# Kernel tuning notes

Hardware: AMD Instinct MI355X
Metric: run time of the kernel (lower is better)

## Reference

```python
import jax, jax.numpy as jnp
import numpy as np

T_STEPS = 100
T_EMB = 16
EPS = 1e-8


def sin_emb(t, dim):
    # sinusoidal_time_embedding: [cos(t*f), sin(t*f)] with f = exp(-log(1e4)*i/half)
    half = dim // 2
    freqs = jnp.exp(-jnp.log(jnp.float32(10000.0)) * jnp.arange(half, dtype=jnp.float32) / half)
    a = t.astype(jnp.float32)[:, None] * freqs[None, :]
    return jnp.concatenate([jnp.cos(a), jnp.sin(a)], axis=-1)


def lstm_layer(x_tbf, W_ih, W_hh, b):
    # x_tbf: [T, B, F]; torch gate order i, f, g, o
    B = x_tbf.shape[1]
    H = W_hh.shape[1]

    def step(carry, x_t):
        h, c = carry
        g = x_t @ W_ih.T + h @ W_hh.T + b
        i, f, gg, o = jnp.split(g, 4, axis=-1)
        c = jax.nn.sigmoid(f) * c + jax.nn.sigmoid(i) * jnp.tanh(gg)
        h = jax.nn.sigmoid(o) * jnp.tanh(c)
        return (h, c), h

    z = jnp.zeros((B, H), x_tbf.dtype)
    (h, c), ys = jax.lax.scan(step, (z, z), x_tbf)
    return ys, h


def _forward(x_hist, x_future, y0, turb_idx, pred_steps, init_noise, turb_emb,
             W_ih0, W_hh0, b_ih0, b_hh0, W_ih1, W_hh1, b_ih1, b_hh1,
             W1, b1, W2, b2, W3, b3):
    betas = jnp.linspace(1e-4, 0.02, T_STEPS).astype(jnp.float32)
    alphas = 1.0 - betas
    alpha_bars = jnp.cumprod(alphas)

    B = x_hist.shape[0]
    emb = turb_emb[turb_idx]  # [B, E]
    eh = jnp.broadcast_to(emb[:, None, :], (B, x_hist.shape[1], emb.shape[1]))
    ef = jnp.broadcast_to(emb[:, None, :], (B, x_future.shape[1], emb.shape[1]))
    xh = jnp.concatenate([x_hist, eh], axis=-1).transpose(1, 0, 2)    # [T_in, B, F+E]
    xf = jnp.concatenate([x_future, ef], axis=-1).transpose(1, 0, 2)  # [P, B, exo+E]

    ys0, _ = lstm_layer(xh, W_ih0, W_hh0, b_ih0 + b_hh0)
    _, enc_out = lstm_layer(ys0, W_ih1, W_hh1, b_ih1 + b_hh1)         # [B, H] = h[-1]

    def mlp(x):
        h = jax.nn.relu(x @ W1.T + b1)
        h = jax.nn.relu(h @ W2.T + b2)
        return h @ W3.T + b3

    def ar_step(prev_y, xs):
        exo_t, step, y_init = xs
        cond = jnp.concatenate([enc_out, exo_t, prev_y], axis=1)  # [B, cond_dim]
        h_e = sin_emb(jnp.full((B,), step), T_EMB)

        def dstep(y, t):
            t_e = sin_emb(jnp.full((B,), t), T_EMB)
            eps_hat = mlp(jnp.concatenate([cond, y, t_e, h_e], axis=1))  # [B,1]
            b_t, a_t, ab_t = betas[t], alphas[t], alpha_bars[t]
            pred_x0 = (y - jnp.sqrt(1.0 - ab_t) * eps_hat) / (jnp.sqrt(ab_t) + EPS)
            mean = (y - b_t / (jnp.sqrt(1.0 - ab_t) + EPS) * eps_hat) / (jnp.sqrt(a_t) + EPS)
            # eval mode -> deterministic sampling: posterior noise term is zero
            return jnp.where(t == 0, pred_x0, mean), None

        y, _ = jax.lax.scan(dstep, y_init, jnp.arange(T_STEPS - 1, -1, -1))
        return y, y[:, 0]

    _, seq = jax.lax.scan(ar_step, y0, (xf, jnp.arange(pred_steps), init_noise))
    return seq.T[:, :, None]  # [B, pred_steps, 1]


def setup_inputs() -> dict:
    key = jax.random.key(0)
    ks = list(jax.random.split(key, 24))
    kit = iter(ks)
    B, T_IN, F_IN, EXO, EMB, PRED, HID, NTURB = 1024, 96, 8, 6, 16, 8, 128, 100
    in0 = F_IN + EMB                 # 24
    cond_dim = HID + EXO + EMB + 1   # 151
    in_mlp = cond_dim + 1 + T_EMB + T_EMB  # 184

    def nrm(shape, s=0.05):
        return jax.random.normal(next(kit), shape, jnp.float32) * s

    return {
        'x_hist': jax.random.normal(next(kit), (B, T_IN, F_IN), jnp.float32),
        'x_future': jax.random.normal(next(kit), (B, PRED, EXO), jnp.float32),
        'y0': jnp.zeros((B, 1), jnp.float32),
        'turb_idx': jax.random.randint(next(kit), (B,), 0, NTURB),
        'pred_steps': PRED,
        'init_noise': jax.random.normal(next(kit), (PRED, B, 1), jnp.float32),
        'turb_emb': nrm((NTURB, EMB), 0.1),
        'W_ih0': nrm((4 * HID, in0)), 'W_hh0': nrm((4 * HID, HID)),
        'b_ih0': jnp.zeros((4 * HID,), jnp.float32), 'b_hh0': jnp.zeros((4 * HID,), jnp.float32),
        'W_ih1': nrm((4 * HID, HID)), 'W_hh1': nrm((4 * HID, HID)),
        'b_ih1': jnp.zeros((4 * HID,), jnp.float32), 'b_hh1': jnp.zeros((4 * HID,), jnp.float32),
        'W1': nrm((HID, in_mlp)), 'b1': jnp.zeros((HID,), jnp.float32),
        'W2': nrm((HID, HID)), 'b2': jnp.zeros((HID,), jnp.float32),
        'W3': nrm((1, HID)), 'b3': jnp.zeros((1,), jnp.float32),
    }


def reference(x_hist, x_future, y0, turb_idx, pred_steps, init_noise, turb_emb,
              W_ih0, W_hh0, b_ih0, b_hh0, W_ih1, W_hh1, b_ih1, b_hh1,
              W1, b1, W2, b2, W3, b3):
    return _forward(x_hist, x_future, y0, turb_idx, pred_steps, init_noise, turb_emb,
                    W_ih0, W_hh0, b_ih0, b_hh0, W_ih1, W_hh1, b_ih1, b_hh1,
                    W1, b1, W2, b2, W3, b3)
```

## Files before the change

kernel.cpp:

```cpp
#include <hip/hip_runtime.h>
#include <hip/hip_fp16.h>
#include <stdint.h>


typedef __attribute__((ext_vector_type(2))) _Float16 half2_t;
typedef __attribute__((ext_vector_type(8))) _Float16 v8h;
typedef __attribute__((ext_vector_type(4))) float v4f;

#define DEV __device__ __forceinline__

DEV uint32_t pack2f(float a, float b) {
  __half ha = __float2half_rn(a), hb = __float2half_rn(b);
  return (uint32_t)__half_as_ushort(ha) | ((uint32_t)__half_as_ushort(hb) << 16);
}

DEV float2 up2(uint32_t u) {
  half2_t h = __builtin_bit_cast(half2_t, u);
  return make_float2((float)h.x, (float)h.y);
}

DEV float fast_ex2(float x) {
#if __has_builtin(__builtin_amdgcn_exp2f)
  return __builtin_amdgcn_exp2f(x);
#else
  return exp2f(x);
#endif
}
DEV float fast_rcp(float x) {
#if __has_builtin(__builtin_amdgcn_rcpf)
  return __builtin_amdgcn_rcpf(x);
#else
  return 1.f / x;
#endif
}
DEV float sigm(float x) { return fast_rcp(1.f + fast_ex2(-1.4426950408889634f * x)); }
DEV float tanh_f(float x) {
  return 2.f * fast_rcp(1.f + fast_ex2(-2.8853900817779268f * x)) - 1.f;
}

DEV uint32_t pk_add(uint32_t a, uint32_t b) {
  return __builtin_bit_cast(uint32_t,
      __builtin_bit_cast(half2_t, a) + __builtin_bit_cast(half2_t, b));
}

DEV uint32_t pk_relufma(uint32_t w, uint32_t y, uint32_t b) {
  half2_t r = __builtin_bit_cast(half2_t, w) * __builtin_bit_cast(half2_t, y) +
              __builtin_bit_cast(half2_t, b);
  half2_t z = {(_Float16)0.f, (_Float16)0.f};
#if __has_builtin(__builtin_elementwise_max)
  r = __builtin_elementwise_max(r, z);
#else
  uint32_t u = __builtin_bit_cast(uint32_t, r);
  uint32_t mask = ((u >> 15) & 1u) * 0xFFFFu | ((u >> 31) & 1u) * 0xFFFF0000u;
  r = __builtin_bit_cast(half2_t, u & ~mask);
#endif
  return __builtin_bit_cast(uint32_t, r);
}

DEV uint32_t pk_max0(uint32_t a) {
  half2_t z = {(_Float16)0.f, (_Float16)0.f};
#if __has_builtin(__builtin_elementwise_max)
  return __builtin_bit_cast(uint32_t,
      __builtin_elementwise_max(__builtin_bit_cast(half2_t, a), z));
#else
  uint32_t mask = ((a >> 15) & 1u) * 0xFFFFu | ((a >> 31) & 1u) * 0xFFFF0000u;
  return a & ~mask;
#endif
}

DEV uint32_t cvtpk(float y) {
#if __has_builtin(__builtin_amdgcn_cvt_pkrtz)
  return __builtin_bit_cast(uint32_t, __builtin_amdgcn_cvt_pkrtz(y, y));
#else
  return pack2f(y, y);
#endif
}

DEV uint32_t cvtpk2(float a, float b) {
#if __has_builtin(__builtin_amdgcn_cvt_pkrtz)
  return __builtin_bit_cast(uint32_t, __builtin_amdgcn_cvt_pkrtz(a, b));
#else
  return pack2f(a, b);
#endif
}

DEV half2_t pk_fma2(uint32_t a, uint32_t b, half2_t c) {
  return __builtin_bit_cast(half2_t, a) * __builtin_bit_cast(half2_t, b) + c;
}

static constexpr size_t OFF_XH  = 0;
static constexpr size_t OFF_W0  = 4718592;
static constexpr size_t OFF_BS0 = 4882432;
static constexpr size_t OFF_W1L = 4884480;
static constexpr size_t OFF_BS1 = 5146624;
static constexpr size_t OFF_W2P = 5148672;
static constexpr size_t OFF_ENC = 5181440;
static constexpr size_t OFF_YS0 = 5705728;
static constexpr size_t OFF_TPJ = 30871552;
static constexpr size_t OFF_HPJ = 30897152;
static constexpr size_t OFF_CC  = 30899200;

__global__ void k_prep_xh(const float* __restrict__ xh, const int* __restrict__ tix,
                          const float* __restrict__ temb, uint32_t* __restrict__ out) {
  int idx = blockIdx.x * 256 + threadIdx.x;
  if (idx >= 96 * 1024 * 12) return;
  int m = idx % 12;
  int tb = idx / 12;
  int b = tb & 1023, t = tb >> 10;
  int k0 = 2 * m, k1 = k0 + 1;
  float v0 = (k0 < 8) ? xh[(b * 96 + t) * 8 + k0] : temb[tix[b] * 16 + (k0 - 8)];
  float v1 = (k1 < 8) ? xh[(b * 96 + t) * 8 + k1] : temb[tix[b] * 16 + (k1 - 8)];
  out[idx] = pack2f(v0, v1);
}

__global__ void k_prep_w(const float* __restrict__ Wih0, const float* __restrict__ Whh0,
                         const float* __restrict__ bih0, const float* __restrict__ bhh0,
                         const float* __restrict__ Wih1, const float* __restrict__ Whh1,
                         const float* __restrict__ bih1, const float* __restrict__ bhh1,
                         const float* __restrict__ W2, const float* __restrict__ W1,
                         uint32_t* __restrict__ w0p, uint32_t* __restrict__ w1p,
                         uint32_t* __restrict__ w2p, float* __restrict__ bs0,
                         float* __restrict__ bs1, uint32_t* __restrict__ tpj,
                         uint32_t* __restrict__ hpj, float2* __restrict__ ccg) {
  int idx = blockIdx.x * 256 + threadIdx.x;
  if (idx < 40960) {
    int w = idx / 5120;
    int r = idx % 5120;
    int T = r / 1280; r %= 1280;
    int f = r / 256;  r %= 256;
    int l = r >> 2, c = r & 3;
    int m = l & 15, qf = l >> 4;
    int g = (m & 3) * 128 + w * 16 + (m >> 2) * 4 + T;
    int k0 = f * 32 + qf * 8 + 2 * c, k1 = k0 + 1;
    float a = (k0 < 24) ? Wih0[g * 24 + k0] : ((k0 < 152) ? Whh0[g * 128 + k0 - 24] : 0.f);
    float b = (k1 < 24) ? Wih0[g * 24 + k1] : ((k1 < 152) ? Whh0[g * 128 + k1 - 24] : 0.f);
    w0p[idx] = pack2f(a, b);
  } else if (idx < 106496) {
    int i = idx - 40960;
    int w = i / 8192;
    int r = i % 8192;
    int T = r / 2048; r %= 2048;
    int f = r / 256;  r %= 256;
    int l = r >> 2, c = r & 3;
    int m = l & 15, qf = l >> 4;
    int g = (m & 3) * 128 + w * 16 + (m >> 2) * 4 + T;
    int k0 = f * 32 + qf * 8 + 2 * c, k1 = k0 + 1;
    float a = (k0 < 128) ? Wih1[g * 128 + k0] : Whh1[g * 128 + k0 - 128];
    float b = (k1 < 128) ? Wih1[g * 128 + k1] : Whh1[g * 128 + k1 - 128];
    w1p[i] = pack2f(a, b);
  } else if (idx < 114688) {
    int i = idx - 106496;
    w2p[i] = pack2f(W2[2 * i], W2[2 * i + 1]);
  } else if (idx < 115200) {
    int i = idx - 114688;
    bs0[i] = bih0[i] + bhh0[i];
  } else if (idx < 115712) {
    int i = idx - 115200;
    bs1[i] = bih1[i] + bhh1[i];
  } else if (idx < 122112) {
    int i = idx - 115712;
    int t = i / 64;
    int r = i % 64;
    int q = r / 16, pi = r % 16;
    int k0 = (pi >> 2) * 32 + q * 8 + (pi & 3) * 2;
    float te[16];
#pragma unroll
    for (int j = 0; j < 8; j++) {
      float f = expf(-logf(10000.f) * (float)j / 8.f);
      float a = (float)t * f;
      te[j] = cosf(a);
      te[j + 8] = sinf(a);
    }
    float s0 = 0.f, s1 = 0.f;
#pragma unroll
    for (int j = 0; j < 16; j++) {
      s0 += W1[k0 * 184 + 152 + j] * te[j];
      s1 += W1[(k0 + 1) * 184 + 152 + j] * te[j];
    }
    tpj[i] = pack2f((float)__half2float(__float2half_rn(s0)),
                    (float)__half2float(__float2half_rn(s1)));
  } else if (idx < 122624) {
    int i = idx - 122112;
    int s = i / 64;
    int kp = i % 64;
    float te[16];
#pragma unroll
    for (int j = 0; j < 8; j++) {
      float f = expf(-logf(10000.f) * (float)j / 8.f);
      float a = (float)s * f;
      te[j] = cosf(a);
      te[j + 8] = sinf(a);
    }
    float s0 = 0.f, s1 = 0.f;
#pragma unroll
    for (int j = 0; j < 16; j++) {
      s0 += W1[(2 * kp) * 184 + 168 + j] * te[j];
      s1 += W1[(2 * kp + 1) * 184 + 168 + j] * te[j];
    }
    hpj[i] = pack2f((float)__half2float(__float2half_rn(s0)),
                    (float)__half2float(__float2half_rn(s1)));
  } else if (idx < 122724) {
    int qq = idx - 122624;
    float ab = 1.f, beta = 0.f;
    for (int i = 0; i <= qq; i++) {
      beta = 1e-4f + (0.02f - 1e-4f) * (float)i / 99.f;
      ab *= (1.f - beta);
    }
    float cs, cd;
    if (qq == 0) { cs = sqrtf(1.f - ab); cd = 1.f / (sqrtf(ab) + 1e-8f); }
    else { cs = beta / (sqrtf(1.f - ab) + 1e-8f); cd = 1.f / (sqrtf(1.f - beta) + 1e-8f); }
    ccg[qq] = make_float2(cs, cd);
  }
}

__global__ __launch_bounds__(512, 2) void k_lstm0(const uint32_t* __restrict__ xh16,
                                                  const uint32_t* __restrict__ w0A,
                                                  const float* __restrict__ bs0,
                                                  __half* __restrict__ ys0) {
  __shared__ __align__(16) __half inb[2][16][160];
  const int tid = threadIdx.x;
  const int w = tid >> 6, l = tid & 63;
  const int n = l & 15, ql = l >> 4;
  const int ju = w * 16 + ql * 4;
  const int bbase = blockIdx.x * 16;

  uint4 Af[4][5];
#pragma unroll
  for (int T = 0; T < 4; T++)
#pragma unroll
    for (int f = 0; f < 5; f++)
      Af[T][f] = ((const uint4*)w0A)[((w * 4 + T) * 5 + f) * 64 + l];
  float bias[4][4];
#pragma unroll
  for (int T = 0; T < 4; T++)
#pragma unroll
    for (int r = 0; r < 4; r++) bias[T][r] = bs0[r * 128 + ju + T];

  for (int i = tid; i < 2560; i += 512) ((uint32_t*)inb)[i] = 0u;
  __syncthreads();
  if (tid < 192) {
    int b = tid / 12, m = tid % 12;
    ((uint32_t*)&inb[0][b][0])[m] = xh16[(0 * 1024 + bbase + b) * 12 + m];
  }
  float cst[4] = {0.f, 0.f, 0.f, 0.f};
  __syncthreads();

  for (int t = 0; t < 96; t++) {
    const int cur = t & 1, nxt = cur ^ 1;
    uint32_t sx = 0;
    int sb = 0, sm = 0;
    if (t < 95 && tid < 192) {
      sb = tid / 12; sm = tid % 12;
      sx = xh16[((t + 1) * 1024 + bbase + sb) * 12 + sm];
    }
    v4f acc[4];
#pragma unroll
    for (int T = 0; T < 4; T++) acc[T] = (v4f){0.f, 0.f, 0.f, 0.f};
#pragma unroll
    for (int f = 0; f < 5; f++) {
      uint4 bu = *(const uint4*)&inb[cur][n][f * 32 + ql * 8];
      v8h Bv = __builtin_bit_cast(v8h, bu);
#pragma unroll
      for (int T = 0; T < 4; T++)
        acc[T] = __builtin_amdgcn_mfma_f32_16x16x32_f16(
            __builtin_bit_cast(v8h, Af[T][f]), Bv, acc[T], 0, 0, 0);
    }
    float hv[4];
#pragma unroll
    for (int T = 0; T < 4; T++) {
      float gi = acc[T][0] + bias[T][0];
      float gf = acc[T][1] + bias[T][1];
      float gg = acc[T][2] + bias[T][2];
      float go = acc[T][3] + bias[T][3];
      float c = sigm(gf) * cst[T] + sigm(gi) * tanh_f(gg);
      cst[T] = c;
      hv[T] = sigm(go) * tanh_f(c);
    }
    uint32_t h01 = pack2f(hv[0], hv[1]), h23 = pack2f(hv[2], hv[3]);
    *(uint2*)&inb[nxt][n][24 + ju] = make_uint2(h01, h23);
    *(uint2*)((__half*)ys0 + (size_t)(t * 1024 + bbase + n) * 128 + ju) = make_uint2(h01, h23);
    if (t < 95 && tid < 192) ((uint32_t*)&inb[nxt][sb][0])[sm] = sx;
    __syncthreads();
  }
}

__global__ __launch_bounds__(512, 2) void k_lstm1(const uint32_t* __restrict__ ys0u,
                                                  const uint32_t* __restrict__ w1A,
                                                  const float* __restrict__ bs1,
                                                  float* __restrict__ enc) {
  __shared__ __align__(16) __half inb[2][16][264];
  const int tid = threadIdx.x;
  const int w = tid >> 6, l = tid & 63;
  const int n = l & 15, ql = l >> 4;
  const int ju = w * 16 + ql * 4;
  const int bbase = blockIdx.x * 16;
  const int sb = tid >> 5, sc = tid & 31;

  uint4 Af[4][8];
#pragma unroll
  for (int T = 0; T < 4; T++)
#pragma unroll
    for (int f = 0; f < 8; f++)
      Af[T][f] = ((const uint4*)w1A)[((w * 4 + T) * 8 + f) * 64 + l];
  float bias[4][4];
#pragma unroll
  for (int T = 0; T < 4; T++)
#pragma unroll
    for (int r = 0; r < 4; r++) bias[T][r] = bs1[r * 128 + ju + T];

  for (int i = tid; i < 4224; i += 512) ((uint32_t*)inb)[i] = 0u;
  __syncthreads();
  {
    uint2 v = ((const uint2*)ys0u)[(size_t)(0 * 1024 + bbase + sb) * 32 + sc];
    *(uint2*)&inb[0][sb][sc * 4] = v;
  }
  float cst[4] = {0.f, 0.f, 0.f, 0.f};
  __syncthreads();

  for (int t = 0; t < 96; t++) {
    const int cur = t & 1, nxt = cur ^ 1;
    uint2 sv = make_uint2(0u, 0u);
    if (t < 95)
      sv = ((const uint2*)ys0u)[(size_t)((t + 1) * 1024 + bbase + sb) * 32 + sc];
    v4f acc[4];
#pragma unroll
    for (int T = 0; T < 4; T++) acc[T] = (v4f){0.f, 0.f, 0.f, 0.f};
#pragma unroll
    for (int f = 0; f < 8; f++) {
      uint4 bu = *(const uint4*)&inb[cur][n][f * 32 + ql * 8];
      v8h Bv = __builtin_bit_cast(v8h, bu);
#pragma unroll
      for (int T = 0; T < 4; T++)
        acc[T] = __builtin_amdgcn_mfma_f32_16x16x32_f16(
            __builtin_bit_cast(v8h, Af[T][f]), Bv, acc[T], 0, 0, 0);
    }
    float hv[4];
#pragma unroll
    for (int T = 0; T < 4; T++) {
      float gi = acc[T][0] + bias[T][0];
      float gf = acc[T][1] + bias[T][1];
      float gg = acc[T][2] + bias[T][2];
      float go = acc[T][3] + bias[T][3];
      float c = sigm(gf) * cst[T] + sigm(gi) * tanh_f(gg);
      cst[T] = c;
      hv[T] = sigm(go) * tanh_f(c);
    }
    *(uint2*)&inb[nxt][n][128 + ju] = make_uint2(pack2f(hv[0], hv[1]), pack2f(hv[2], hv[3]));
    if (t < 95) *(uint2*)&inb[nxt][sb][sc * 4] = sv;
    if (t == 95)
      *(float4*)&enc[(size_t)(bbase + n) * 128 + ju] = make_float4(hv[0], hv[1], hv[2], hv[3]);
    __syncthreads();
  }
}

__global__ __launch_bounds__(128, 1) void k_diff(
    const float* __restrict__ xfut, const float* __restrict__ y0,
    const int* __restrict__ tix, const float* __restrict__ noise,
    const float* __restrict__ temb, const float* __restrict__ W1,
    const float* __restrict__ b1, const float* __restrict__ b2,
    const float* __restrict__ W3, const float* __restrict__ b3,
    const uint32_t* __restrict__ w2p, const float* __restrict__ enc,
    const uint32_t* __restrict__ tpj, const uint32_t* __restrict__ hpj,
    const float2* __restrict__ ccG, float* __restrict__ out) {
  __shared__ uint32_t W1sL[128 * 65];
  __shared__ uint32_t W1xL[128 * 29];
  __shared__ uint32_t encPL[16 * 65];
  __shared__ uint32_t embPL[16 * 9];
  __shared__ uint32_t encdL[128 * 17];
  __shared__ __align__(16) float partL[2][16][12];

  const int tid = threadIdx.x;
  const int w = tid >> 6, l = tid & 63;
  const int m = l & 15, q = l >> 4;
  const int gbase = blockIdx.x * 16;
  const uint4* tpj4 = (const uint4*)tpj;

  for (int i = tid; i < 128 * 64; i += 128) {
    int r = i >> 6, c = i & 63;
    W1sL[r * 65 + c] = pack2f(W1[r * 184 + 2 * c], W1[r * 184 + 2 * c + 1]);
  }
  for (int i = tid; i < 128 * 28; i += 128) {
    int r = i / 28, c = i % 28;
    W1xL[r * 29 + c] = pack2f(W1[r * 184 + 128 + 2 * c], W1[r * 184 + 129 + 2 * c]);
  }
  for (int i = tid; i < 16 * 64; i += 128) {
    int bq = i >> 6, c = i & 63;
    encPL[bq * 65 + c] = pack2f(enc[(gbase + bq) * 128 + 2 * c],
                                enc[(gbase + bq) * 128 + 2 * c + 1]);
  }
  for (int i = tid; i < 16 * 8; i += 128) {
    int bq = i >> 3, c = i & 7;
    const float* er = temb + tix[gbase + bq] * 16;
    embPL[bq * 9 + c] = pack2f(er[2 * c], er[2 * c + 1]);
  }
  __syncthreads();

  for (int pi = 0; pi < 16; pi++) {
    int k0 = (pi >> 2) * 32 + q * 8 + (pi & 3) * 2;
    half2_t a0 = {(_Float16)0.f, (_Float16)0.f};
    half2_t a1 = a0;
    const uint32_t* wr0 = &W1sL[k0 * 65];
    const uint32_t* wr1 = &W1sL[(k0 + 1) * 65];
    const uint32_t* ep = &encPL[m * 65];
#pragma unroll 8
    for (int c = 0; c < 64; c++) {
      half2_t e = __builtin_bit_cast(half2_t, ep[c]);
      a0 += __builtin_bit_cast(half2_t, wr0[c]) * e;
      a1 += __builtin_bit_cast(half2_t, wr1[c]) * e;
    }
#pragma unroll
    for (int c = 0; c < 8; c++) {
      half2_t e = __builtin_bit_cast(half2_t, embPL[m * 9 + c]);
      a0 += __builtin_bit_cast(half2_t, W1xL[k0 * 29 + 3 + c]) * e;
      a1 += __builtin_bit_cast(half2_t, W1xL[(k0 + 1) * 29 + 3 + c]) * e;
    }
    float e0 = b1[k0] + (float)a0.x + (float)a0.y;
    float e1 = b1[k0 + 1] + (float)a1.x + (float)a1.y;
    encdL[tid * 17 + pi] = pack2f(e0, e1);
  }

  uint4 Bf[4][4];
  {
    const uint4* w2u4 = (const uint4*)w2p;
#pragma unroll
    for (int j = 0; j < 4; j++)
#pragma unroll
      for (int f = 0; f < 4; f++)
        Bf[j][f] = w2u4[((4 * w + j) * 16 + m) * 16 + f * 4 + q];
  }
  uint32_t b2P[8], w3P[8];
#pragma unroll
  for (int j = 0; j < 4; j++) {
    int tt = 4 * w + j;
    b2P[2 * j]     = pack2f(b2[tt * 16 + q * 4 + 0], b2[tt * 16 + q * 4 + 1]);
    b2P[2 * j + 1] = pack2f(b2[tt * 16 + q * 4 + 2], b2[tt * 16 + q * 4 + 3]);
    w3P[2 * j]     = pack2f(W3[tt * 16 + q * 4 + 0], W3[tt * 16 + q * 4 + 1]);
    w3P[2 * j + 1] = pack2f(W3[tt * 16 + q * 4 + 2], W3[tt * 16 + q * 4 + 3]);
  }
  const float b3v = b3[0];
  const int pslot = w * 4 + q;

  uint32_t w1yP[16];
#pragma unroll
  for (int pi = 0; pi < 16; pi++) {
    int k0 = (pi >> 2) * 32 + q * 8 + (pi & 3) * 2;
    uint32_t ua = W1xL[k0 * 29 + 11];
    uint32_t ub = W1xL[(k0 + 1) * 29 + 11];
    w1yP[pi] = (ua >> 16) | (ub & 0xFFFF0000u);
  }

  float prev_y = y0[gbase + m];
  __syncthreads();

  float y = 0.f;
  float2 ccv = make_float2(0.f, 0.f);
  uint32_t bph[16], bt[16];
  const v4f zf = (v4f){0.f, 0.f, 0.f, 0.f};

#define DSTEP(t_, PB)                                                          \
  do {                                                                         \
    const int tn_ = ((t_) > 0) ? (t_) - 1 : 0;                                 \
    const uint4* tg_ = tpj4 + (size_t)(tn_ * 4 + q) * 4;    \
    uint4 t0 = tg_[0], t1 = tg_[1], t2 = tg_[2], t3 = tg_[3];                  \
    float2 ccn_ = ccG[tn_];                                                    \
    const uint32_t yP = cvtpk(y);                                              \
    uint4 au[4];                                                               \
    _Pragma("unroll")                                                          \
    for (int f = 0; f < 4; f++) {                                              \
      au[f].x = pk_relufma(w1yP[4 * f + 0], yP, bt[4 * f + 0]);                \
      au[f].y = pk_relufma(w1yP[4 * f + 1], yP, bt[4 * f + 1]);                \
      au[f].z = pk_relufma(w1yP[4 * f + 2], yP, bt[4 * f + 2]);                \
      au[f].w = pk_relufma(w1yP[4 * f + 3], yP, bt[4 * f + 3]);                \
    }                                                                          \
                            \
    v4f aA[4], aB[4];                                                          \
    _Pragma("unroll")                                                          \
    for (int j = 0; j < 4; j++)                                                \
      aA[j] = __builtin_amdgcn_mfma_f32_16x16x32_f16(                          \
          __builtin_bit_cast(v8h, Bf[j][0]), __builtin_bit_cast(v8h, au[0]),   \
          zf, 0, 0, 0);                                                        \
    _Pragma("unroll")                                                          \
    for (int j = 0; j < 4; j++)                                                \
      aB[j] = __builtin_amdgcn_mfma_f32_16x16x32_f16(                          \
          __builtin_bit_cast(v8h, Bf[j][1]), __builtin_bit_cast(v8h, au[1]),   \
          zf, 0, 0, 0);                                                        \
    _Pragma("unroll")                                                          \
    for (int j = 0; j < 4; j++)                                                \
      aA[j] = __builtin_amdgcn_mfma_f32_16x16x32_f16(                          \
          __builtin_bit_cast(v8h, Bf[j][2]), __builtin_bit_cast(v8h, au[2]),   \
          aA[j], 0, 0, 0);                                                     \
    _Pragma("unroll")                                                          \
    for (int j = 0; j < 4; j++)                                                \
      aB[j] = __builtin_amdgcn_mfma_f32_16x16x32_f16(                          \
          __builtin_bit_cast(v8h, Bf[j][3]), __builtin_bit_cast(v8h, au[3]),   \
          aB[j], 0, 0, 0);                                                     \
              \
    half2_t runA = {(_Float16)0.f, (_Float16)0.f};                             \
    half2_t runB = runA;                                                       \
    _Pragma("unroll")                                                          \
    for (int j = 0; j < 2; j++) {                                              \
      v4f c = aA[j] + aB[j];                                                   \
      uint32_t h01 = pk_max0(pk_add(cvtpk2(c[0], c[1]), b2P[2 * j]));          \
      uint32_t h23 = pk_max0(pk_add(cvtpk2(c[2], c[3]), b2P[2 * j + 1]));      \
      runA = pk_fma2(h01, w3P[2 * j], runA);                                   \
      runA = pk_fma2(h23, w3P[2 * j + 1], runA);                               \
    }                                                                          \
    _Pragma("unroll")                                                          \
    for (int j = 2; j < 4; j++) {                                              \
      v4f c = aA[j] + aB[j];                                                   \
      uint32_t h01 = pk_max0(pk_add(cvtpk2(c[0], c[1]), b2P[2 * j]));          \
      uint32_t h23 = pk_max0(pk_add(cvtpk2(c[2], c[3]), b2P[2 * j + 1]));      \
      runB = pk_fma2(h01, w3P[2 * j], runB);                                   \
      runB = pk_fma2(h23, w3P[2 * j + 1], runB);                               \
    }                                                                          \
    partL[PB][m][pslot] = ((float)runA.x + (float)runA.y) +                    \
                          ((float)runB.x + (float)runB.y);                     \
                                         \
    bt[0] = pk_add(bph[0], t0.x);   bt[1] = pk_add(bph[1], t0.y);              \
    bt[2] = pk_add(bph[2], t0.z);   bt[3] = pk_add(bph[3], t0.w);              \
    bt[4] = pk_add(bph[4], t1.x);   bt[5] = pk_add(bph[5], t1.y);              \
    bt[6] = pk_add(bph[6], t1.z);   bt[7] = pk_add(bph[7], t1.w);              \
    bt[8] = pk_add(bph[8], t2.x);   bt[9] = pk_add(bph[9], t2.y);              \
    bt[10] = pk_add(bph[10], t2.z); bt[11] = pk_add(bph[11], t2.w);            \
    bt[12] = pk_add(bph[12], t3.x); bt[13] = pk_add(bph[13], t3.y);            \
    bt[14] = pk_add(bph[14], t3.z); bt[15] = pk_add(bph[15], t3.w);            \
    __syncthreads();                                                           \
    const v4f* pl_ = (const v4f*)&partL[PB][m][0];                             \
    v4f ps_ = pl_[0] + pl_[1];                                                 \
    float eps_ = b3v + ((ps_[0] + ps_[1]) + (ps_[2] + ps_[3]));                \
    y = (y - ccv.x * eps_) * ccv.y;                                            \
    ccv = ccn_;                                                                \
  } while (0)

  for (int s = 0; s < 8; s++) {
    float yn = noise[s * 1024 + gbase + m];
    float xf[6];
#pragma unroll
    for (int i = 0; i < 6; i++) xf[i] = xfut[((gbase + m) * 8 + s) * 6 + i];
#pragma unroll
    for (int pi = 0; pi < 16; pi++) {
      int k0 = (pi >> 2) * 32 + q * 8 + (pi & 3) * 2;
      float2 ed = up2(encdL[tid * 17 + pi]);
      float e0 = ed.x, e1 = ed.y;
#pragma unroll
      for (int c = 0; c < 3; c++) {
        float2 w0v = up2(W1xL[k0 * 29 + c]);
        float2 w1v = up2(W1xL[(k0 + 1) * 29 + c]);
        e0 += w0v.x * xf[2 * c] + w0v.y * xf[2 * c + 1];
        e1 += w1v.x * xf[2 * c] + w1v.y * xf[2 * c + 1];
      }
      e0 += up2(W1xL[k0 * 29 + 11]).x * prev_y;
      e1 += up2(W1xL[(k0 + 1) * 29 + 11]).x * prev_y;
      float2 hh = up2(hpj[s * 64 + (k0 >> 1)]);
      e0 += hh.x;
      e1 += hh.y;
      bph[pi] = pack2f(e0, e1);
    }

    y = yn;
    {
      const uint4* tg = tpj4 + (size_t)(99 * 4 + q) * 4;
      uint4 t0 = tg[0], t1 = tg[1], t2 = tg[2], t3 = tg[3];
      bt[0] = pk_add(bph[0], t0.x);   bt[1] = pk_add(bph[1], t0.y);
      bt[2] = pk_add(bph[2], t0.z);   bt[3] = pk_add(bph[3], t0.w);
      bt[4] = pk_add(bph[4], t1.x);   bt[5] = pk_add(bph[5], t1.y);
      bt[6] = pk_add(bph[6], t1.z);   bt[7] = pk_add(bph[7], t1.w);
      bt[8] = pk_add(bph[8], t2.x);   bt[9] = pk_add(bph[9], t2.y);
      bt[10] = pk_add(bph[10], t2.z); bt[11] = pk_add(bph[11], t2.w);
      bt[12] = pk_add(bph[12], t3.x); bt[13] = pk_add(bph[13], t3.y);
      bt[14] = pk_add(bph[14], t3.z); bt[15] = pk_add(bph[15], t3.w);
    }
    ccv = ccG[99];

    for (int it = 0; it < 50; it++) {
      DSTEP(99 - 2 * it, 0);
      DSTEP(98 - 2 * it, 1);
    }

    if (w == 0 && l < 16) out[(gbase + l) * 8 + s] = y;
    prev_y = y;
  }
#undef DSTEP
}

extern "C" void kernel_launch(void* const* d_in, const int* in_sizes, int n_in,
                              void* d_out, int out_size, void* d_ws, size_t ws_size,
                              hipStream_t stream) {
  const float* x_hist    = (const float*)d_in[0];
  const float* x_future  = (const float*)d_in[1];
  const float* y0        = (const float*)d_in[2];
  const int*   turb_idx  = (const int*)d_in[3];
  const float* init_noise = (const float*)d_in[5];
  const float* turb_emb  = (const float*)d_in[6];
  const float* W_ih0     = (const float*)d_in[7];
  const float* W_hh0     = (const float*)d_in[8];
  const float* b_ih0     = (const float*)d_in[9];
  const float* b_hh0     = (const float*)d_in[10];
  const float* W_ih1     = (const float*)d_in[11];
  const float* W_hh1     = (const float*)d_in[12];
  const float* b_ih1     = (const float*)d_in[13];
  const float* b_hh1     = (const float*)d_in[14];
  const float* W1        = (const float*)d_in[15];
  const float* b1        = (const float*)d_in[16];
  const float* W2        = (const float*)d_in[17];
  const float* b2        = (const float*)d_in[18];
  const float* W3        = (const float*)d_in[19];
  const float* b3        = (const float*)d_in[20];

  char* ws = (char*)d_ws;
  uint32_t* xh16 = (uint32_t*)(ws + OFF_XH);
  uint32_t* w0p  = (uint32_t*)(ws + OFF_W0);
  float*    bs0  = (float*)(ws + OFF_BS0);
  uint32_t* w1p  = (uint32_t*)(ws + OFF_W1L);
  float*    bs1  = (float*)(ws + OFF_BS1);
  uint32_t* w2p  = (uint32_t*)(ws + OFF_W2P);
  float*    encf = (float*)(ws + OFF_ENC);
  __half*   ys0h = (__half*)(ws + OFF_YS0);
  uint32_t* tpjw = (uint32_t*)(ws + OFF_TPJ);
  uint32_t* hpjw = (uint32_t*)(ws + OFF_HPJ);
  float2*   ccw  = (float2*)(ws + OFF_CC);

  k_prep_xh<<<4608, 256, 0, stream>>>(x_hist, turb_idx, turb_emb, xh16);
  k_prep_w<<<480, 256, 0, stream>>>(W_ih0, W_hh0, b_ih0, b_hh0,
                                    W_ih1, W_hh1, b_ih1, b_hh1,
                                    W2, W1, w0p, w1p, w2p, bs0, bs1,
                                    tpjw, hpjw, ccw);
  k_lstm0<<<64, 512, 0, stream>>>(xh16, w0p, bs0, ys0h);
  k_lstm1<<<64, 512, 0, stream>>>((const uint32_t*)ys0h, w1p, bs1, encf);
  k_diff<<<64, 128, 0, stream>>>(x_future, y0, turb_idx, init_noise, turb_emb,
                                 W1, b1, b2, W3, b3, w2p, encf,
                                 tpjw, hpjw, ccw, (float*)d_out);
}
```

Measured before the change: 702.0 us.

## Split diffusion MLP output tiles across four waves and fold step coefficients

The diffusion kernel moves from 2 to 4 waves per block. Each wave now computes 2 of the 8 output column tiles of the second MLP layer instead of 4, which halves the serial MFMA chain and the register footprint per wave, with partial sums reduced through a wider shared buffer. The update coefficients are also prefolded (cs*cd), so the y update is a precomputed term minus a scaled sum and work moves off the post-barrier critical path. The cost is more waves joining each per-step barrier and a 16-way shared-memory reduction instead of 8-way.

New measurement: 633.2 us (median of 2 runs). 9.8% less time.

```diff
diff --git a/kernel.cpp b/kernel.cpp
--- a/kernel.cpp
+++ b/kernel.cpp
@@ -209,7 +209,7 @@
     float cs, cd;
     if (qq == 0) { cs = sqrtf(1.f - ab); cd = 1.f / (sqrtf(ab) + 1e-8f); }
     else { cs = beta / (sqrtf(1.f - ab) + 1e-8f); cd = 1.f / (sqrtf(1.f - beta) + 1e-8f); }
-    ccg[qq] = make_float2(cs, cd);
+    ccg[qq] = make_float2(cs * cd, cd);
   }
 }
 
@@ -353,7 +353,7 @@
   }
 }
 
-__global__ __launch_bounds__(128, 1) void k_diff(
+__global__ __launch_bounds__(256, 1) void k_diff(
     const float* __restrict__ xfut, const float* __restrict__ y0,
     const int* __restrict__ tix, const float* __restrict__ noise,
     const float* __restrict__ temb, const float* __restrict__ W1,
@@ -366,8 +366,8 @@
   __shared__ uint32_t W1xL[128 * 29];
   __shared__ uint32_t encPL[16 * 65];
   __shared__ uint32_t embPL[16 * 9];
-  __shared__ uint32_t encdL[128 * 17];
-  __shared__ __align__(16) float partL[2][16][12];
+  __shared__ uint32_t encdL[256 * 17];
+  __shared__ __align__(16) float partL[2][16][20];
 
   const int tid = threadIdx.x;
   const int w = tid >> 6, l = tid & 63;
@@ -375,20 +375,20 @@
   const int gbase = blockIdx.x * 16;
   const uint4* tpj4 = (const uint4*)tpj;
 
-  for (int i = tid; i < 128 * 64; i += 128) {
+  for (int i = tid; i < 128 * 64; i += 256) {
     int r = i >> 6, c = i & 63;
     W1sL[r * 65 + c] = pack2f(W1[r * 184 + 2 * c], W1[r * 184 + 2 * c + 1]);
   }
-  for (int i = tid; i < 128 * 28; i += 128) {
+  for (int i = tid; i < 128 * 28; i += 256) {
     int r = i / 28, c = i % 28;
     W1xL[r * 29 + c] = pack2f(W1[r * 184 + 128 + 2 * c], W1[r * 184 + 129 + 2 * c]);
   }
-  for (int i = tid; i < 16 * 64; i += 128) {
+  for (int i = tid; i < 16 * 64; i += 256) {
     int bq = i >> 6, c = i & 63;
     encPL[bq * 65 + c] = pack2f(enc[(gbase + bq) * 128 + 2 * c],
                                 enc[(gbase + bq) * 128 + 2 * c + 1]);
   }
-  for (int i = tid; i < 16 * 8; i += 128) {
+  for (int i = tid; i < 16 * 8; i += 256) {
     int bq = i >> 3, c = i & 7;
     const float* er = temb + tix[gbase + bq] * 16;
     embPL[bq * 9 + c] = pack2f(er[2 * c], er[2 * c + 1]);
@@ -419,19 +419,19 @@
     encdL[tid * 17 + pi] = pack2f(e0, e1);
   }
 
-  uint4 Bf[4][4];
+  uint4 Bf[2][4];
   {
     const uint4* w2u4 = (const uint4*)w2p;
 #pragma unroll
-    for (int j = 0; j < 4; j++)
+    for (int j = 0; j < 2; j++)
 #pragma unroll
       for (int f = 0; f < 4; f++)
-        Bf[j][f] = w2u4[((4 * w + j) * 16 + m) * 16 + f * 4 + q];
-  }
-  uint32_t b2P[8], w3P[8];
-#pragma unroll
-  for (int j = 0; j < 4; j++) {
-    int tt = 4 * w + j;
+        Bf[j][f] = w2u4[((2 * w + j) * 16 + m) * 16 + f * 4 + q];
+  }
+  uint32_t b2P[4], w3P[4];
+#pragma unroll
+  for (int j = 0; j < 2; j++) {
+    int tt = 2 * w + j;
     b2P[2 * j]     = pack2f(b2[tt * 16 + q * 4 + 0], b2[tt * 16 + q * 4 + 1]);
     b2P[2 * j + 1] = pack2f(b2[tt * 16 + q * 4 + 2], b2[tt * 16 + q * 4 + 3]);
     w3P[2 * j]     = pack2f(W3[tt * 16 + q * 4 + 0], W3[tt * 16 + q * 4 + 1]);
@@ -462,7 +462,7 @@
     const int tn_ = ((t_) > 0) ? (t_) - 1 : 0;                                 \
     const uint4* tg_ = tpj4 + (size_t)(tn_ * 4 + q) * 4;    \
     uint4 t0 = tg_[0], t1 = tg_[1], t2 = tg_[2], t3 = tg_[3];                  \
-    float2 ccn_ = ccG[tn_];                                                    \
+    float2 cck_ = ccG[tn_];                                                    \
     const uint32_t yP = cvtpk(y);                                              \
     uint4 au[4];                                                               \
     _Pragma("unroll")                                                          \
@@ -472,50 +472,44 @@
       au[f].z = pk_relufma(w1yP[4 * f + 2], yP, bt[4 * f + 2]);                \
       au[f].w = pk_relufma(w1yP[4 * f + 3], yP, bt[4 * f + 3]);                \
     }                                                                          \
-                            \
-    v4f aA[4], aB[4];                                                          \
-    _Pragma("unroll")                                                          \
-    for (int j = 0; j < 4; j++)                                                \
-      aA[j] = __builtin_amdgcn_mfma_f32_16x16x32_f16(                          \
-          __builtin_bit_cast(v8h, Bf[j][0]), __builtin_bit_cast(v8h, au[0]),   \
-          zf, 0, 0, 0);                                                        \
-    _Pragma("unroll")                                                          \
-    for (int j = 0; j < 4; j++)                                                \
-      aB[j] = __builtin_amdgcn_mfma_f32_16x16x32_f16(                          \
-          __builtin_bit_cast(v8h, Bf[j][1]), __builtin_bit_cast(v8h, au[1]),   \
-          zf, 0, 0, 0);                                                        \
-    _Pragma("unroll")                                                          \
-    for (int j = 0; j < 4; j++)                                                \
-      aA[j] = __builtin_amdgcn_mfma_f32_16x16x32_f16(                          \
-          __builtin_bit_cast(v8h, Bf[j][2]), __builtin_bit_cast(v8h, au[2]),   \
-          aA[j], 0, 0, 0);                                                     \
-    _Pragma("unroll")                                                          \
-    for (int j = 0; j < 4; j++)                                                \
-      aB[j] = __builtin_amdgcn_mfma_f32_16x16x32_f16(                          \
-          __builtin_bit_cast(v8h, Bf[j][3]), __builtin_bit_cast(v8h, au[3]),   \
-          aB[j], 0, 0, 0);                                                     \
-              \
+                             \
+    v4f a0 = __builtin_amdgcn_mfma_f32_16x16x32_f16(                           \
+        __builtin_bit_cast(v8h, Bf[0][0]), __builtin_bit_cast(v8h, au[0]), zf, 0, 0, 0); \
+    v4f b0 = __builtin_amdgcn_mfma_f32_16x16x32_f16(                           \
+        __builtin_bit_cast(v8h, Bf[0][1]), __builtin_bit_cast(v8h, au[1]), zf, 0, 0, 0); \
+    v4f a1 = __builtin_amdgcn_mfma_f32_16x16x32_f16(                           \
+        __builtin_bit_cast(v8h, Bf[1][0]), __builtin_bit_cast(v8h, au[0]), zf, 0, 0, 0); \
+    v4f b1x = __builtin_amdgcn_mfma_f32_16x16x32_f16(                          \
+        __builtin_bit_cast(v8h, Bf[1][1]), __builtin_bit_cast(v8h, au[1]), zf, 0, 0, 0); \
+    a0 = __builtin_amdgcn_mfma_f32_16x16x32_f16(                               \
+        __builtin_bit_cast(v8h, Bf[0][2]), __builtin_bit_cast(v8h, au[2]), a0, 0, 0, 0); \
+    b0 = __builtin_amdgcn_mfma_f32_16x16x32_f16(                               \
+        __builtin_bit_cast(v8h, Bf[0][3]), __builtin_bit_cast(v8h, au[3]), b0, 0, 0, 0); \
+    a1 = __builtin_amdgcn_mfma_f32_16x16x32_f16(                               \
+        __builtin_bit_cast(v8h, Bf[1][2]), __builtin_bit_cast(v8h, au[2]), a1, 0, 0, 0); \
+    b1x = __builtin_amdgcn_mfma_f32_16x16x32_f16(                              \
+        __builtin_bit_cast(v8h, Bf[1][3]), __builtin_bit_cast(v8h, au[3]), b1x, 0, 0, 0); \
+    v4f c0 = a0 + b0, c1 = a1 + b1x;                                           \
+                      \
     half2_t runA = {(_Float16)0.f, (_Float16)0.f};                             \
     half2_t runB = runA;                                                       \
-    _Pragma("unroll")                                                          \
-    for (int j = 0; j < 2; j++) {                                              \
-      v4f c = aA[j] + aB[j];                                                   \
-      uint32_t h01 = pk_max0(pk_add(cvtpk2(c[0], c[1]), b2P[2 * j]));          \
-      uint32_t h23 = pk_max0(pk_add(cvtpk2(c[2], c[3]), b2P[2 * j + 1]));      \
-      runA = pk_fma2(h01, w3P[2 * j], runA);                                   \
-      runA = pk_fma2(h23, w3P[2 * j + 1], runA);                               \
-    }                                                                          \
-    _Pragma("unroll")                                                          \
-    for (int j = 2; j < 4; j++) {                                              \
-      v4f c = aA[j] + aB[j];                                                   \
-      uint32_t h01 = pk_max0(pk_add(cvtpk2(c[0], c[1]), b2P[2 * j]));          \
-      uint32_t h23 = pk_max0(pk_add(cvtpk2(c[2], c[3]), b2P[2 * j + 1]));      \
-      runB = pk_fma2(h01, w3P[2 * j], runB);                                   \
-      runB = pk_fma2(h23, w3P[2 * j + 1], runB);                               \
+    {                                                                          \
+      uint32_t h01 = pk_max0(pk_add(cvtpk2(c0[0], c0[1]), b2P[0]));            \
+      uint32_t h23 = pk_max0(pk_add(cvtpk2(c0[2], c0[3]), b2P[1]));            \
+      runA = pk_fma2(h01, w3P[0], runA);                                       \
+      runA = pk_fma2(h23, w3P[1], runA);                                       \
+      uint32_t g01 = pk_max0(pk_add(cvtpk2(c1[0], c1[1]), b2P[2]));            \
+      uint32_t g23 = pk_max0(pk_add(cvtpk2(c1[2], c1[3]), b2P[3]));            \
+      runB = pk_fma2(g01, w3P[2], runB);                                       \
+      runB = pk_fma2(g23, w3P[3], runB);                                       \
     }                                                                          \
     partL[PB][m][pslot] = ((float)runA.x + (float)runA.y) +                    \
                           ((float)runB.x + (float)runB.y);                     \
-                                         \
+    const float pre_ = ccv.y * y - ccv.x * b3v;           \
+    __syncthreads();                                                           \
+               \
+    const v4f* pl_ = (const v4f*)&partL[PB][m][0];                             \
+    v4f p0_ = pl_[0], p1_ = pl_[1], p2_ = pl_[2], p3_ = pl_[3];                \
     bt[0] = pk_add(bph[0], t0.x);   bt[1] = pk_add(bph[1], t0.y);              \
     bt[2] = pk_add(bph[2], t0.z);   bt[3] = pk_add(bph[3], t0.w);              \
     bt[4] = pk_add(bph[4], t1.x);   bt[5] = pk_add(bph[5], t1.y);              \
@@ -524,12 +518,9 @@
     bt[10] = pk_add(bph[10], t2.z); bt[11] = pk_add(bph[11], t2.w);            \
     bt[12] = pk_add(bph[12], t3.x); bt[13] = pk_add(bph[13], t3.y);            \
     bt[14] = pk_add(bph[14], t3.z); bt[15] = pk_add(bph[15], t3.w);            \
-    __syncthreads();                                                           \
-    const v4f* pl_ = (const v4f*)&partL[PB][m][0];                             \
-    v4f ps_ = pl_[0] + pl_[1];                                                 \
-    float eps_ = b3v + ((ps_[0] + ps_[1]) + (ps_[2] + ps_[3]));                \
-    y = (y - ccv.x * eps_) * ccv.y;                                            \
-    ccv = ccn_;                                                                \
+    v4f ps_ = (p0_ + p1_) + (p2_ + p3_);                                       \
+    y = pre_ - ccv.x * ((ps_[0] + ps_[1]) + (ps_[2] + ps_[3]));                \
+    ccv = cck_;                                                                \
   } while (0)
 
   for (int s = 0; s < 8; s++) {
@@ -627,7 +618,7 @@
                                     tpjw, hpjw, ccw);
   k_lstm0<<<64, 512, 0, stream>>>(xh16, w0p, bs0, ys0h);
   k_lstm1<<<64, 512, 0, stream>>>((const uint32_t*)ys0h, w1p, bs1, encf);
-  k_diff<<<64, 128, 0, stream>>>(x_future, y0, turb_idx, init_noise, turb_emb,
+  k_diff<<<64, 256, 0, stream>>>(x_future, y0, turb_idx, init_noise, turb_emb,
                                  W1, b1, b2, W3, b3, w2p, encf,
                                  tpjw, hpjw, ccw, (float*)d_out);
 }
```
